# Kernel tuning notes

Measured on AMD Instinct MI355X. Metric: run time of the kernel, lower is better.

## Reference

```python
import jax, jax.numpy as jnp
import numpy as np

S = 14       # grid size
B = 2        # boxes per cell
C = 20       # classes
N_EL = B * 5 + C   # 30
L_COORD = 5.0
L_NOOBJ = 0.5
BATCH = 4096
NBOX = 16


def setup_inputs() -> dict:
    key = jax.random.key(0)
    k1, k2, k3, k4 = jax.random.split(key, 4)
    prediction = jax.random.uniform(k1, (BATCH, S * S * N_EL), dtype=jnp.float32)
    # well-formed ground-truth boxes: centers in (0.05,0.95), sizes in (0.02,0.3)
    cxcy = jax.random.uniform(k2, (BATCH, NBOX, 2), minval=0.05, maxval=0.95, dtype=jnp.float32)
    wh = jax.random.uniform(k3, (BATCH, NBOX, 2), minval=0.02, maxval=0.3, dtype=jnp.float32)
    boxes = jnp.concatenate([cxcy - wh / 2, cxcy + wh / 2], axis=-1)  # x1,y1,x2,y2
    classes = jax.random.randint(k4, (BATCH, NBOX), 0, C, dtype=jnp.int32)
    return {"prediction": prediction, "boxes": boxes, "classes": classes}


def _encode(boxes, classes):
    """Vectorized version of YoloLoss.encode: scatter boxes into SxS grid cells.
    Faithful detail: class one-hot goes to channel 9+class (the original's
    off-by-one: class 0 lands on the 2nd confidence channel)."""
    bsz, nbox = classes.shape
    cell = 1.0 / S
    xy1, xy2 = boxes[..., :2], boxes[..., 2:]
    wh = xy2 - xy1
    cxcy = (xy1 + xy2) / 2
    ij = jnp.clip(jnp.ceil(cxcy / cell) - 1, 0, S - 1)          # [b,nbox,2] (x,y)
    dxy = cxcy / cell - ij                                      # delta inside cell
    ij = ij.astype(jnp.int32)
    one = jnp.ones_like(wh[..., :1])
    zcls = jnp.zeros(classes.shape + (C,), dtype=boxes.dtype)
    # layout: [dxy, wh, conf, dxy, wh, conf, class one-hots]
    base = jnp.concatenate([dxy, wh, one, dxy, wh, one, zcls], axis=-1)  # [b,nbox,30]
    cls_oh = jax.nn.one_hot(classes + (B * 5 - 1), N_EL, dtype=boxes.dtype)  # index 9+class
    vec = jnp.maximum(base, cls_oh)
    flat_idx = (jnp.arange(bsz, dtype=jnp.int32)[:, None] * (S * S)
                + ij[..., 1] * S + ij[..., 0]).reshape(-1)      # row-major (y,x)
    target = jnp.zeros((bsz * S * S, N_EL), dtype=boxes.dtype)
    return target.at[flat_idx].set(vec.reshape(-1, N_EL))


def _pairwise_iou(a, b):
    """a,b: [N,B,4] -> iou [N,B(pred),B(target)] (corner-format jaccard, as in
    the original, applied to (dx,dy,w,h) rows verbatim)."""
    a4 = a[:, :, None, :]
    b4 = b[:, None, :, :]
    lt = jnp.maximum(a4[..., :2], b4[..., :2])
    rb = jnp.minimum(a4[..., 2:], b4[..., 2:])
    whi = jnp.clip(rb - lt, 0.0)
    inter = whi[..., 0] * whi[..., 1]
    area_a = (a4[..., 2] - a4[..., 0]) * (a4[..., 3] - a4[..., 1])
    area_b = (b4[..., 2] - b4[..., 0]) * (b4[..., 3] - b4[..., 1])
    union = area_a + area_b - inter
    return inter / jnp.where(union == 0, 1.0, union)


def reference(prediction, boxes, classes):
    target = _encode(boxes, classes)                       # [bsz*S*S, 30]
    pred = prediction.reshape(-1, N_EL)
    coord = target[:, 4] > 0                               # cells containing objects
    coordf = coord.astype(pred.dtype)
    noobjf = (target[:, 4] == 0).astype(pred.dtype)

    conf_idx = jnp.array([4, 9])
    noobj_loss = jnp.sum(noobjf[:, None] * (pred[:, conf_idx] - target[:, conf_idx]) ** 2)
    class_loss = jnp.sum(coordf[:, None] * (pred[:, B * 5:] - target[:, B * 5:]) ** 2)

    bp = pred[:, :B * 5].reshape(-1, B, 5)                 # [N,B,5]
    bt = target[:, :B * 5].reshape(-1, B, 5)

    iou = _pairwise_iou(bp[..., :4], bt[..., :4])          # [N,B,B]
    max_index = jnp.argmax(iou, axis=1)                    # best pred per target box
    response = (max_index[:, None, :] == jnp.arange(B)[None, :, None]).any(-1)  # [N,B]
    resp = response & coord[:, None]
    respf = resp.astype(pred.dtype)

    contain_loss = jnp.sum(respf * (bp[..., 4] - bt[..., 4]) ** 2)
    bt_wh = jnp.where(resp[..., None], bt[..., 2:4], 1.0)  # guard sqrt at masked cells
    loc_loss = jnp.sum(respf * (((bp[..., :2] - bt[..., :2]) ** 2).sum(-1)
                                + ((jnp.sqrt(bp[..., 2:4]) - jnp.sqrt(bt_wh)) ** 2).sum(-1)))

    return L_COORD * loc_loss + contain_loss + L_NOOBJ * noobj_loss + class_loss
```

## Files before the change

kernel.cpp:

```cpp
#include <hip/hip_runtime.h>


#define SGRID 14
#define CELLS 196
#define NEL 30
#define NBOX 16
#define PRED_PER_BATCH 5880
#define VEC_PER_ROW 1470
#define STREAM_ITERS 12
#define STREAM_TPB 256
#define STREAM_CHUNK (STREAM_ITERS * STREAM_TPB)
#define ROWS_PER_OBJ_BLOCK 16
#define OBJ_TILE (ROWS_PER_OBJ_BLOCK * CELLS)

typedef float v4f __attribute__((ext_vector_type(4)));

__global__ __launch_bounds__(256) void yolo_fused_kernel(
    const v4f*    __restrict__ pred4,
    const float4* __restrict__ boxes,
    const int*    __restrict__ classes,
    float* __restrict__ partials,
    int nvec, int nrows, int objblocks)
{
    __shared__ int s_win[OBJ_TILE];

    const int tid = threadIdx.x;
    const int bid = blockIdx.x;
    const int v0  = bid * STREAM_CHUNK;
    const float cellw = (float)(1.0 / 14.0);
    const bool isobj = bid < objblocks;

    float4 bx; int cls = 0;
    const int row = bid * ROWS_PER_OBJ_BLOCK + (tid >> 4);
    const int k   = tid & 15;
    const bool has_box = isobj && row < nrows;
    if (has_box) {
        bx  = boxes[row * NBOX + k];
        cls = classes[row * NBOX + k];
    }

    float loss = 0.0f;
    const bool full = (v0 + STREAM_CHUNK) <= nvec;

    v4f vv[STREAM_ITERS];
    if (full) {
        #pragma unroll
        for (int i = 0; i < STREAM_ITERS; ++i)
            vv[i] = pred4[v0 + tid + i * STREAM_TPB];
    }

    if (isobj) {
        #pragma unroll
        for (int i = 0; i < (OBJ_TILE + STREAM_TPB - 1) / STREAM_TPB; ++i) {
            int idx = tid + i * STREAM_TPB;
            if (idx < OBJ_TILE) s_win[idx] = -1;
        }
        __syncthreads();
        float dx, dy, bw, bh; int cell = 0;
        if (has_box) {
            bw = bx.z - bx.x;  bh = bx.w - bx.y;
            float cx = (bx.x + bx.z) * 0.5f, cy = (bx.y + bx.w) * 0.5f;
            float fx = cx / cellw, fy = cy / cellw;
            float fi = fminf(fmaxf(ceilf(fx) - 1.0f, 0.0f), 13.0f);
            float fj = fminf(fmaxf(ceilf(fy) - 1.0f, 0.0f), 13.0f);
            dx = fx - fi;  dy = fy - fj;
            cell = (int)fj * SGRID + (int)fi;
            atomicMax(&s_win[(tid >> 4) * CELLS + cell], (k << 8) | (9 + cls));
        }
        __syncthreads();
        if (has_box) {
            int wv = s_win[(tid >> 4) * CELLS + cell];
            if ((wv >> 8) == k) {
                const float* p = (const float*)pred4 + (size_t)(row * CELLS + cell) * NEL;
                int hot = wv & 0xFF;
                float a[10];
                #pragma unroll
                for (int j = 0; j < 5; ++j) {
                    float2 t = *(const float2*)(p + 2 * j);
                    a[2 * j] = t.x;  a[2 * j + 1] = t.y;
                }
                float csum = 0.0f;
                #pragma unroll
                for (int j = 0; j < 10; ++j) {
                    float2 t = *(const float2*)(p + 10 + 2 * j);
                    float d0 = t.x - ((10 + 2 * j) == hot ? 1.0f : 0.0f);
                    float d1 = t.y - ((11 + 2 * j) == hot ? 1.0f : 0.0f);
                    csum += d0 * d0 + d1 * d1;
                }
                loss += csum;
                loss -= 0.5f * (a[4] * a[4] + a[9] * a[9]);
                float area_t = (bw - dx) * (bh - dy);
                float iou[2];
                #pragma unroll
                for (int i = 0; i < 2; ++i) {
                    const float* q = a + i * 5;
                    float ltx = fmaxf(q[0], dx), lty = fmaxf(q[1], dy);
                    float rbx = fminf(q[2], bw), rby = fminf(q[3], bh);
                    float wi = fmaxf(rbx - ltx, 0.0f);
                    float hi = fmaxf(rby - lty, 0.0f);
                    float inter  = wi * hi;
                    float area_a = (q[2] - q[0]) * (q[3] - q[1]);
                    float uni    = area_a + area_t - inter;
                    iou[i] = inter / ((uni == 0.0f) ? 1.0f : uni);
                }
                int r = (iou[1] > iou[0]) ? 1 : 0;
                const float* q = a + r * 5;
                float dc = q[4] - 1.0f;
                loss += dc * dc;
                float lx = q[0] - dx, ly = q[1] - dy;
                float lw = sqrtf(q[2]) - sqrtf(bw);
                float lh = sqrtf(q[3]) - sqrtf(bh);
                loss += 5.0f * (lx * lx + ly * ly + lw * lw + lh * lh);
            }
        }
    }

    if (full) {
        int g0 = (v0 + tid) * 4;
        int c  = (int)((unsigned)g0 / 30u);
        int c0 = g0 - c * 30;
        #pragma unroll
        for (int i = 0; i < STREAM_ITERS; ++i) {
            v4f v = vv[i];
            #pragma unroll
            for (int j = 0; j < 4; ++j) {
                int cj = c0 + j;
                int cc = (cj >= 30) ? cj - 30 : cj;
                float wgt = ((cc == 4) | (cc == 9)) ? 0.5f : 0.0f;
                loss = fmaf(wgt * v[j], v[j], loss);
            }
            c0 += 4;  if (c0 >= 30) c0 -= 30;
        }
    } else {
        for (int i = 0; i < STREAM_ITERS; ++i) {
            int e = v0 + tid + i * STREAM_TPB;
            if (e < nvec) {
                v4f v = pred4[e];
                int g = e * 4;
                int c = (int)((unsigned)g / 30u);
                int c0 = g - c * 30;
                #pragma unroll
                for (int j = 0; j < 4; ++j) {
                    int cj = c0 + j;
                    int cc = (cj >= 30) ? cj - 30 : cj;
                    float wgt = ((cc == 4) | (cc == 9)) ? 0.5f : 0.0f;
                    loss = fmaf(wgt * v[j], v[j], loss);
                }
            }
        }
    }

    #pragma unroll
    for (int off = 32; off > 0; off >>= 1)
        loss += __shfl_down(loss, off, 64);
    if ((tid & 63) == 0)
        partials[bid * 4 + (tid >> 6)] = loss;
}

__global__ __launch_bounds__(1024) void final_reduce_kernel(
    const float* __restrict__ partials, float* __restrict__ out, int n)
{
    float s = 0.0f;
    #pragma unroll 4
    for (int i = threadIdx.x; i < n; i += 1024) s += partials[i];
    #pragma unroll
    for (int off = 32; off > 0; off >>= 1)
        s += __shfl_down(s, off, 64);
    __shared__ float w16[16];
    if ((threadIdx.x & 63) == 0) w16[threadIdx.x >> 6] = s;
    __syncthreads();
    if (threadIdx.x < 64) {
        float t = (threadIdx.x < 16) ? w16[threadIdx.x] : 0.0f;
        #pragma unroll
        for (int off = 8; off > 0; off >>= 1)
            t += __shfl_down(t, off, 64);
        if (threadIdx.x == 0) out[0] = t;
    }
}

extern "C" void kernel_launch(void* const* d_in, const int* in_sizes, int n_in,
                              void* d_out, int out_size, void* d_ws, size_t ws_size,
                              hipStream_t stream) {
    const float* pred    = (const float*)d_in[0];
    const float* boxes   = (const float*)d_in[1];
    const int*   classes = (const int*)d_in[2];
    float* out = (float*)d_out;

    const int nrows = in_sizes[0] / PRED_PER_BATCH;
    const int nvec  = nrows * PRED_PER_BATCH / 4;
    const int sblocks   = (nvec + STREAM_CHUNK - 1) / STREAM_CHUNK;
    const int objblocks = (nrows + ROWS_PER_OBJ_BLOCK - 1) / ROWS_PER_OBJ_BLOCK;

    float* partials = (float*)d_ws;

    yolo_fused_kernel<<<dim3(sblocks), dim3(STREAM_TPB), 0, stream>>>(
        (const v4f*)pred, (const float4*)boxes, classes, partials,
        nvec, nrows, objblocks);
    final_reduce_kernel<<<dim3(1), dim3(1024), 0, stream>>>(partials, out, sblocks * 4);
}
```

Before: 144.4 us.

## Load only confidence channels per cell instead of streaming full prediction tensor

Replaces the full vectorized stream over every prediction element with strided scalar loads of channels 4 and 9 per cell, since only those contribute to the no-object term. This is meant to cut DRAM traffic, because the other channels of non-object cells are never needed. The grid shrinks to 8 cells per thread, and the reduction unroll is tweaked. The cost is uncoalesced strided access, where each cell's two values may touch separate sectors, and fewer blocks to hide latency.

After: 145.2 us. About the same (+0.5%).

```diff
diff --git a/kernel.cpp b/kernel.cpp
--- a/kernel.cpp
+++ b/kernel.cpp
@@ -6,27 +6,23 @@
 #define NEL 30
 #define NBOX 16
 #define PRED_PER_BATCH 5880
-#define VEC_PER_ROW 1470
-#define STREAM_ITERS 12
 #define STREAM_TPB 256
-#define STREAM_CHUNK (STREAM_ITERS * STREAM_TPB)
+#define CPT 8
+#define SCELLS (CPT * STREAM_TPB)
 #define ROWS_PER_OBJ_BLOCK 16
 #define OBJ_TILE (ROWS_PER_OBJ_BLOCK * CELLS)
 
-typedef float v4f __attribute__((ext_vector_type(4)));
-
 __global__ __launch_bounds__(256) void yolo_fused_kernel(
-    const v4f*    __restrict__ pred4,
+    const float*  __restrict__ pred,
     const float4* __restrict__ boxes,
     const int*    __restrict__ classes,
     float* __restrict__ partials,
-    int nvec, int nrows, int objblocks)
+    int ncells, int nrows, int objblocks)
 {
     __shared__ int s_win[OBJ_TILE];
 
     const int tid = threadIdx.x;
     const int bid = blockIdx.x;
-    const int v0  = bid * STREAM_CHUNK;
     const float cellw = (float)(1.0 / 14.0);
     const bool isobj = bid < objblocks;
 
@@ -39,15 +35,26 @@
         cls = classes[row * NBOX + k];
     }
 
+    const int cbase = bid * SCELLS + tid;
+    float v4a[CPT], v9a[CPT];
+    if (bid * SCELLS + SCELLS <= ncells) {
+        #pragma unroll
+        for (int i = 0; i < CPT; ++i) {
+            const float* r = pred + (size_t)(cbase + i * STREAM_TPB) * NEL;
+            v4a[i] = r[4];  v9a[i] = r[9];
+        }
+    } else {
+        #pragma unroll
+        for (int i = 0; i < CPT; ++i) {
+            int c = cbase + i * STREAM_TPB;
+            if (c < ncells) {
+                const float* r = pred + (size_t)c * NEL;
+                v4a[i] = r[4];  v9a[i] = r[9];
+            } else { v4a[i] = 0.0f; v9a[i] = 0.0f; }
+        }
+    }
+
     float loss = 0.0f;
-    const bool full = (v0 + STREAM_CHUNK) <= nvec;
-
-    v4f vv[STREAM_ITERS];
-    if (full) {
-        #pragma unroll
-        for (int i = 0; i < STREAM_ITERS; ++i)
-            vv[i] = pred4[v0 + tid + i * STREAM_TPB];
-    }
 
     if (isobj) {
         #pragma unroll
@@ -71,7 +78,7 @@
         if (has_box) {
             int wv = s_win[(tid >> 4) * CELLS + cell];
             if ((wv >> 8) == k) {
-                const float* p = (const float*)pred4 + (size_t)(row * CELLS + cell) * NEL;
+                const float* p = pred + (size_t)(row * CELLS + cell) * NEL;
                 int hot = wv & 0xFF;
                 float a[10];
                 #pragma unroll
@@ -115,39 +122,10 @@
         }
     }
 
-    if (full) {
-        int g0 = (v0 + tid) * 4;
-        int c  = (int)((unsigned)g0 / 30u);
-        int c0 = g0 - c * 30;
-        #pragma unroll
-        for (int i = 0; i < STREAM_ITERS; ++i) {
-            v4f v = vv[i];
-            #pragma unroll
-            for (int j = 0; j < 4; ++j) {
-                int cj = c0 + j;
-                int cc = (cj >= 30) ? cj - 30 : cj;
-                float wgt = ((cc == 4) | (cc == 9)) ? 0.5f : 0.0f;
-                loss = fmaf(wgt * v[j], v[j], loss);
-            }
-            c0 += 4;  if (c0 >= 30) c0 -= 30;
-        }
-    } else {
-        for (int i = 0; i < STREAM_ITERS; ++i) {
-            int e = v0 + tid + i * STREAM_TPB;
-            if (e < nvec) {
-                v4f v = pred4[e];
-                int g = e * 4;
-                int c = (int)((unsigned)g / 30u);
-                int c0 = g - c * 30;
-                #pragma unroll
-                for (int j = 0; j < 4; ++j) {
-                    int cj = c0 + j;
-                    int cc = (cj >= 30) ? cj - 30 : cj;
-                    float wgt = ((cc == 4) | (cc == 9)) ? 0.5f : 0.0f;
-                    loss = fmaf(wgt * v[j], v[j], loss);
-                }
-            }
-        }
+    #pragma unroll
+    for (int i = 0; i < CPT; ++i) {
+        loss = fmaf(0.5f * v4a[i], v4a[i], loss);
+        loss = fmaf(0.5f * v9a[i], v9a[i], loss);
     }
 
     #pragma unroll
@@ -161,7 +139,7 @@
     const float* __restrict__ partials, float* __restrict__ out, int n)
 {
     float s = 0.0f;
-    #pragma unroll 4
+    #pragma unroll 2
     for (int i = threadIdx.x; i < n; i += 1024) s += partials[i];
     #pragma unroll
     for (int off = 32; off > 0; off >>= 1)
@@ -186,15 +164,15 @@
     const int*   classes = (const int*)d_in[2];
     float* out = (float*)d_out;
 
-    const int nrows = in_sizes[0] / PRED_PER_BATCH;
-    const int nvec  = nrows * PRED_PER_BATCH / 4;
-    const int sblocks   = (nvec + STREAM_CHUNK - 1) / STREAM_CHUNK;
+    const int nrows  = in_sizes[0] / PRED_PER_BATCH;
+    const int ncells = nrows * CELLS;
+    int sblocks = (ncells + SCELLS - 1) / SCELLS;
     const int objblocks = (nrows + ROWS_PER_OBJ_BLOCK - 1) / ROWS_PER_OBJ_BLOCK;
+    if (sblocks < objblocks) sblocks = objblocks;
 
     float* partials = (float*)d_ws;
 
     yolo_fused_kernel<<<dim3(sblocks), dim3(STREAM_TPB), 0, stream>>>(
-        (const v4f*)pred, (const float4*)boxes, classes, partials,
-        nvec, nrows, objblocks);
+        pred, (const float4*)boxes, classes, partials, ncells, nrows, objblocks);
     final_reduce_kernel<<<dim3(1), dim3(1024), 0, stream>>>(partials, out, sblocks * 4);
 }
```
